# Kernel tuning notes

Hardware: AMD Instinct MI355X
Metric: run time of the kernel (lower is better)

Reference implementation:

```python
import jax, jax.numpy as jnp
import numpy as np

D = 1024; DI = 2048; DS = 16; DTR = 64; K = 4          # mamba dims
HR = 16; DHR = 64                                       # rwkv heads
HA = 32; DHA = 32                                       # attention heads
NM = 6; NR = 4; NT = 2                                  # layer counts
B = 2; L = 1024


def _rms(x, w):
    return x * jax.lax.rsqrt(jnp.mean(x * x, axis=-1, keepdims=True) + 1e-6) * w


def _dwconv(x, w, b):
    # causal depthwise conv over seq; x [B,L,DI], w [K,1,DI]
    xp = jnp.pad(x, ((0, 0), (K - 1, 0), (0, 0)))
    y = jax.lax.conv_general_dilated(xp, w, (1,), 'VALID',
        dimension_numbers=('NWC', 'WIO', 'NWC'), feature_group_count=DI)
    return y + b


def _selective_scan(u, delta, A, Bm, Cm):
    # u,delta [B,L,DI]; A [DI,DS]; Bm,Cm [B,L,DS]
    def step(h, inp):
        u_t, d_t, b_t, c_t = inp
        dA = jnp.exp(d_t[:, :, None] * A)                     # [B,DI,DS]
        h = h * dA + (d_t * u_t)[:, :, None] * b_t[:, None, :]
        return h, jnp.einsum('bds,bs->bd', h, c_t)
    h0 = jnp.zeros((u.shape[0], DI, DS), u.dtype)
    tm = lambda a: jnp.swapaxes(a, 0, 1)                      # time-major
    _, ys = jax.lax.scan(step, h0, (tm(u), tm(delta), tm(Bm), tm(Cm)))
    return jnp.swapaxes(ys, 0, 1)


def _mamba(x, p):
    norm, Win, cw, cb, Wx, Wdt, bdt, Alog, Dp, Wout = p
    xn = _rms(x, norm)
    xz = xn @ Win                                             # [B,L,2*DI]
    xc, z = jnp.split(xz, 2, axis=-1)
    xc = jax.nn.silu(_dwconv(xc, cw, cb))
    xdbl = xc @ Wx                                            # [B,L,DTR+2*DS]
    dt = xdbl[..., :DTR]
    Bm = xdbl[..., DTR:DTR + DS]
    Cm = xdbl[..., DTR + DS:]
    delta = jax.nn.softplus(dt @ Wdt + bdt)                   # [B,L,DI]
    A = -jnp.exp(Alog)
    y = _selective_scan(xc, delta, A, Bm, Cm) + Dp * xc
    y = y * jax.nn.silu(z)
    return x + y @ Wout


def _rwkv(x, p):
    norm, mu, Wr, Wk, Wv, Wo, wlog, u = p
    Bb, Ll = x.shape[0], x.shape[1]
    xn = _rms(x, norm)
    xs = jnp.pad(xn, ((0, 0), (1, 0), (0, 0)))[:, :-1, :]     # token shift
    mix = lambda m: xn * m + xs * (1.0 - m)
    r = (mix(mu[0]) @ Wr).reshape(Bb, Ll, HR, DHR)
    k = (mix(mu[1]) @ Wk).reshape(Bb, Ll, HR, DHR)
    v = (mix(mu[2]) @ Wv).reshape(Bb, Ll, HR, DHR)
    w = jnp.exp(-jnp.exp(wlog))                               # decay in (0,1)
    def step(S, inp):
        r_t, k_t, v_t = inp                                   # [B,HR,DHR]
        kv = jnp.einsum('bhk,bhv->bhkv', k_t, v_t)
        y = jnp.einsum('bhk,bhkv->bhv', r_t, S + u[None, :, :, None] * kv)
        return w[None, :, :, None] * S + kv, y
    S0 = jnp.zeros((Bb, HR, DHR, DHR), x.dtype)
    tm = lambda a: jnp.swapaxes(a, 0, 1)
    _, ys = jax.lax.scan(step, S0, (tm(r), tm(k), tm(v)))
    y = jnp.swapaxes(ys, 0, 1).reshape(Bb, Ll, D)
    return x + y @ Wo


def _mha(x, p):
    Wq, bq, Wk, bk, Wv, bv, Wo, bo = p
    q = jnp.einsum('bld,dhk->blhk', x, Wq) + bq
    k = jnp.einsum('bld,dhk->blhk', x, Wk) + bk
    v = jnp.einsum('bld,dhk->blhk', x, Wv) + bv
    scale = 1.0 / float(np.sqrt(DHA))
    att = jax.nn.softmax(jnp.einsum('blhk,bmhk->bhlm', q, k) * scale, axis=-1)
    o = jnp.einsum('bhlm,bmhk->blhk', att, v)
    return jnp.einsum('blhk,hkd->bld', o, Wo) + bo


def setup_inputs() -> dict:
    key = jax.random.key(0)
    ks = iter(jax.random.split(key, 40))
    nrm = lambda s, sc=0.02: jax.random.normal(next(ks), s, jnp.float32) * sc
    return {
        'x': jax.random.normal(next(ks), (B, L, D), jnp.float32),
        'm_norm': jnp.ones((NM, D), jnp.float32),
        'm_Win': nrm((NM, D, 2 * DI)),
        'm_conv_w': nrm((NM, K, 1, DI)),
        'm_conv_b': jnp.zeros((NM, DI), jnp.float32),
        'm_Wx': nrm((NM, DI, DTR + 2 * DS)),
        'm_Wdt': nrm((NM, DTR, DI)),
        'm_bdt': jnp.full((NM, DI), -4.6, jnp.float32),
        'm_Alog': jnp.broadcast_to(jnp.log(jnp.arange(1, DS + 1, dtype=jnp.float32)), (NM, DI, DS)) + jnp.zeros((NM, DI, DS), jnp.float32),
        'm_D': jnp.ones((NM, DI), jnp.float32),
        'm_Wout': nrm((NM, DI, D)),
        'r_norm': jnp.ones((NR, D), jnp.float32),
        'r_mu': jax.random.uniform(next(ks), (NR, 3, D), jnp.float32),
        'r_Wr': nrm((NR, D, D)), 'r_Wk': nrm((NR, D, D)),
        'r_Wv': nrm((NR, D, D)), 'r_Wo': nrm((NR, D, D)),
        'r_wlog': nrm((NR, HR, DHR), 0.5),
        'r_u': nrm((NR, HR, DHR), 0.5),
        'a_Wq': nrm((NT, D, HA, DHA)), 'a_bq': jnp.zeros((NT, HA, DHA), jnp.float32),
        'a_Wk': nrm((NT, D, HA, DHA)), 'a_bk': jnp.zeros((NT, HA, DHA), jnp.float32),
        'a_Wv': nrm((NT, D, HA, DHA)), 'a_bv': jnp.zeros((NT, HA, DHA), jnp.float32),
        'a_Wo': nrm((NT, HA, DHA, D)), 'a_bo': jnp.zeros((NT, D), jnp.float32),
        'f_W': nrm((3 * D, 3)), 'f_b': jnp.zeros((3,), jnp.float32),
    }


def reference(x, m_norm, m_Win, m_conv_w, m_conv_b, m_Wx, m_Wdt, m_bdt, m_Alog, m_D, m_Wout,
              r_norm, r_mu, r_Wr, r_Wk, r_Wv, r_Wo, r_wlog, r_u,
              a_Wq, a_bq, a_Wk, a_bk, a_Wv, a_bv, a_Wo, a_bo, f_W, f_b):
    m = x
    for i in range(NM):
        m = _mamba(m, (m_norm[i], m_Win[i], m_conv_w[i], m_conv_b[i], m_Wx[i],
                       m_Wdt[i], m_bdt[i], m_Alog[i], m_D[i], m_Wout[i]))
    r = x
    for i in range(NR):
        r = _rwkv(r, (r_norm[i], r_mu[i], r_Wr[i], r_Wk[i], r_Wv[i], r_Wo[i],
                      r_wlog[i], r_u[i]))
    t = x
    for i in range(NT):
        t = _mha(t, (a_Wq[i], a_bq[i], a_Wk[i], a_bk[i], a_Wv[i], a_bv[i],
                     a_Wo[i], a_bo[i]))
    combined = jnp.concatenate([m, r, t], axis=-1)           # [B,L,3*D]
    return jax.nn.softmax(combined @ f_W + f_b, axis=-1)     # [B,L,3]
```

## Files before the change

### kernel.cpp

```cpp
#include <hip/hip_runtime.h>
#include <hip/hip_bf16.h>
#include <cstddef>

#define D_   1024
#define DI_  2048
#define DS_  16
#define DTR_ 64
#define KC_  4
#define HR_  16
#define DHR_ 64
#define HA_  32
#define DHA_ 32
#define NM_  6
#define NR_  4
#define NT_  2
#define B_   2
#define L_   1024
#define NBL  (B_*L_)

typedef __hip_bfloat16 bf16;
typedef __attribute__((ext_vector_type(8))) short short8v;
typedef __attribute__((ext_vector_type(4))) float float4v;

__device__ __forceinline__ float bfbits2f(unsigned short u) {
    return __uint_as_float(((unsigned int)u) << 16);
}
__device__ __forceinline__ float b2f(bf16 x) { return __bfloat162float(x); }
__device__ __forceinline__ unsigned short f2bfbits(float f) {
    bf16 h = __float2bfloat16(f);
    return *reinterpret_cast<unsigned short*>(&h);
}
__device__ __forceinline__ float ldf(const void* p, long i, int bf) {
    if (bf) return bfbits2f(((const unsigned short*)p)[i]);
    return ((const float*)p)[i];
}
__device__ __forceinline__ float softplus_f(float x) {
    return x > 20.f ? x : log1pf(__expf(x));
}
__device__ __forceinline__ float silu_f(float x) {
    return x / (1.f + __expf(-x));
}

__global__ __launch_bounds__(256) void diag_k(float* __restrict__ out, float code)
{
    const int idx = blockIdx.x * 256 + threadIdx.x;
    if (idx < NBL * 3) out[idx] = (idx == 0 ? code : 0.f);
}

__global__ __launch_bounds__(64) void detect_k(const void* __restrict__ x,
                                               int* __restrict__ flag)
{
    const unsigned short* u = (const unsigned short*)x;
    int local = 0;
    for (int i = threadIdx.x; i < 1024; i += 64) {
        const float av = fabsf(bfbits2f(u[i]));
        if (!(av < 1e6f)) local = 1;
    }
    const unsigned long long b = __ballot(local);
    if (threadIdx.x == 0) flag[0] = b ? 0 : 1;
}

#define BM 64
#define BN 64
#define TK 64
#define LDT 72

__global__ __launch_bounds__(256) void gemm_big_k(
    const void* __restrict__ A, int lda, int aDt,
    const void* __restrict__ W, long woff,
    const void* __restrict__ bias, long boff, int hasBias,
    void* __restrict__ C, int ldc, int cDt,
    int N, int K, int act, int acc,
    const int* __restrict__ flagp)
{
    const int bf = *flagp;
    __shared__ short As[128 * LDT];
    __shared__ short Bs[128 * LDT];
    const int bm = blockIdx.y * 128;
    const int bn = blockIdx.x * 128;
    const int tid = threadIdx.x;
    const int lane = tid & 63;
    const int wid = tid >> 6;
    const int wr = wid >> 1, wc = wid & 1;

    const int fc  = lane & 15;
    const int g   = lane >> 4;
    const int fk8 = g << 3;

    const int sa_row = tid >> 1;
    const int sa_k   = (tid & 1) << 5;

    const int sb_n = tid & 127;
    const int sb_k = (tid >> 7) << 5;

    float4v accv[4][4] = {};

    for (int k0 = 0; k0 < K; k0 += TK) {
        if (aDt) {
            const unsigned short* ap = (const unsigned short*)A
                + (size_t)(bm + sa_row) * lda + k0 + sa_k;
            #pragma unroll
            for (int q = 0; q < 4; ++q)
                *(short8v*)&As[sa_row * LDT + sa_k + q * 8] =
                    *(const short8v*)(ap + q * 8);
        } else {
            const float* ap = (const float*)A + (size_t)(bm + sa_row) * lda + k0 + sa_k;
            #pragma unroll
            for (int q = 0; q < 4; ++q) {
                const float4 v0 = *(const float4*)(ap + q * 8);
                const float4 v1 = *(const float4*)(ap + q * 8 + 4);
                short8v t;
                t[0]=(short)f2bfbits(v0.x); t[1]=(short)f2bfbits(v0.y);
                t[2]=(short)f2bfbits(v0.z); t[3]=(short)f2bfbits(v0.w);
                t[4]=(short)f2bfbits(v1.x); t[5]=(short)f2bfbits(v1.y);
                t[6]=(short)f2bfbits(v1.z); t[7]=(short)f2bfbits(v1.w);
                *(short8v*)&As[sa_row * LDT + sa_k + q * 8] = t;
            }
        }
        {
            const long wbase = woff + (long)(k0 + sb_k) * N + (bn + sb_n);
            short tmp[32];
            if (bf) {
                const unsigned short* wp = (const unsigned short*)W;
                #pragma unroll
                for (int j = 0; j < 32; ++j) tmp[j] = (short)wp[wbase + (long)j * N];
            } else {
                const float* wp = (const float*)W;
                #pragma unroll
                for (int j = 0; j < 32; ++j) tmp[j] = (short)f2bfbits(wp[wbase + (long)j * N]);
            }
            #pragma unroll
            for (int q = 0; q < 4; ++q) {
                short8v t;
                #pragma unroll
                for (int e = 0; e < 8; ++e) t[e] = tmp[q * 8 + e];
                *(short8v*)&Bs[sb_n * LDT + sb_k + q * 8] = t;
            }
        }
        __syncthreads();
        #pragma unroll
        for (int ks = 0; ks < TK; ks += 32) {
            short8v af[4], bfr[4];
            #pragma unroll
            for (int mi = 0; mi < 4; ++mi)
                af[mi] = *(const short8v*)&As[(wr * 64 + mi * 16 + fc) * LDT + ks + fk8];
            #pragma unroll
            for (int ni = 0; ni < 4; ++ni)
                bfr[ni] = *(const short8v*)&Bs[(wc * 64 + ni * 16 + fc) * LDT + ks + fk8];
            #pragma unroll
            for (int mi = 0; mi < 4; ++mi)
                #pragma unroll
                for (int ni = 0; ni < 4; ++ni)
                    accv[mi][ni] = __builtin_amdgcn_mfma_f32_16x16x32_bf16(
                        af[mi], bfr[ni], accv[mi][ni], 0, 0, 0);
        }
        __syncthreads();
    }

    const int crow0 = bm + wr * 64 + (g << 2);
    const int ccol0 = bn + wc * 64 + fc;
    #pragma unroll
    for (int ni = 0; ni < 4; ++ni) {
        const int col = ccol0 + ni * 16;
        if (col < N) {
            const float bsv = hasBias ? ldf(bias, boff + col, bf) : 0.f;
            #pragma unroll
            for (int mi = 0; mi < 4; ++mi) {
                #pragma unroll
                for (int j = 0; j < 4; ++j) {
                    const int row = crow0 + mi * 16 + j;
                    float r = accv[mi][ni][j] + bsv;
                    if (act == 1) r = softplus_f(r);
                    if (cDt) {
                        ((bf16*)C)[(size_t)row * ldc + col] = __float2bfloat16(r);
                    } else {
                        float* cp = (float*)C + (size_t)row * ldc + col;
                        if (acc) r += *cp;
                        *cp = r;
                    }
                }
            }
        }
    }
}

__global__ __launch_bounds__(256) void gemm_k(
    const void* __restrict__ A, int lda, int aDt,
    const void* __restrict__ W, long woff,
    const void* __restrict__ bias, long boff, int hasBias,
    void* __restrict__ C, int ldc, int cDt,
    int N, int K, int act, int acc,
    const int* __restrict__ flagp)
{
    const int bf = *flagp;
    __shared__ short As[BM * LDT];
    __shared__ short Bs[BN * LDT];
    const int bm = blockIdx.y * BM;
    const int bn = blockIdx.x * BN;
    const int tid = threadIdx.x;
    const int lane = tid & 63;
    const int wid = tid >> 6;
    const int wr = wid >> 1, wc = wid & 1;

    const int sa_row = tid >> 2;
    const int sa_kq  = (tid & 3) << 4;
    const int sb_col = tid & 63;
    const int sb_kq  = (tid >> 6) << 4;
    const int sb_gn  = bn + sb_col;

    float4v accv[2][2] = {};

    for (int k0 = 0; k0 < K; k0 += TK) {
        {
            short8v a0, a1;
            const size_t aoff = (size_t)(bm + sa_row) * lda + k0 + sa_kq;
            if (aDt) {
                a0 = *(const short8v*)((const unsigned short*)A + aoff);
                a1 = *(const short8v*)((const unsigned short*)A + aoff + 8);
            } else {
                const float* ap = (const float*)A + aoff;
                const float4 v0 = *(const float4*)(ap + 0);
                const float4 v1 = *(const float4*)(ap + 4);
                const float4 v2 = *(const float4*)(ap + 8);
                const float4 v3 = *(const float4*)(ap + 12);
                a0[0]=f2bfbits(v0.x); a0[1]=f2bfbits(v0.y); a0[2]=f2bfbits(v0.z); a0[3]=f2bfbits(v0.w);
                a0[4]=f2bfbits(v1.x); a0[5]=f2bfbits(v1.y); a0[6]=f2bfbits(v1.z); a0[7]=f2bfbits(v1.w);
                a1[0]=f2bfbits(v2.x); a1[1]=f2bfbits(v2.y); a1[2]=f2bfbits(v2.z); a1[3]=f2bfbits(v2.w);
                a1[4]=f2bfbits(v3.x); a1[5]=f2bfbits(v3.y); a1[6]=f2bfbits(v3.z); a1[7]=f2bfbits(v3.w);
            }
            *(short8v*)&As[sa_row * LDT + sa_kq + 0] = a0;
            *(short8v*)&As[sa_row * LDT + sa_kq + 8] = a1;
        }
        {
            short8v b0, b1;
            #pragma unroll
            for (int j = 0; j < 8; ++j) { b0[j] = 0; b1[j] = 0; }
            if (sb_gn < N) {
                const long wbase = woff + (long)(k0 + sb_kq) * N + sb_gn;
                if (bf) {
                    const unsigned short* wp = (const unsigned short*)W;
                    #pragma unroll
                    for (int j = 0; j < 8; ++j) {
                        b0[j] = (short)wp[wbase + (long)j * N];
                        b1[j] = (short)wp[wbase + (long)(j + 8) * N];
                    }
                } else {
                    const float* wp = (const float*)W;
                    #pragma unroll
                    for (int j = 0; j < 8; ++j) {
                        b0[j] = (short)f2bfbits(wp[wbase + (long)j * N]);
                        b1[j] = (short)f2bfbits(wp[wbase + (long)(j + 8) * N]);
                    }
                }
            }
            *(short8v*)&Bs[sb_col * LDT + sb_kq + 0] = b0;
            *(short8v*)&Bs[sb_col * LDT + sb_kq + 8] = b1;
        }
        __syncthreads();
        {
            const int r  = lane & 15;
            const int kb = (lane >> 4) << 3;
            #pragma unroll
            for (int ks = 0; ks < TK; ks += 32) {
                const int kg = ks + kb;
                const short8v a0 = *(const short8v*)&As[(wr*32 +      r) * LDT + kg];
                const short8v a1 = *(const short8v*)&As[(wr*32 + 16 + r) * LDT + kg];
                const short8v b0 = *(const short8v*)&Bs[(wc*32 +      r) * LDT + kg];
                const short8v b1 = *(const short8v*)&Bs[(wc*32 + 16 + r) * LDT + kg];
                accv[0][0] = __builtin_amdgcn_mfma_f32_16x16x32_bf16(a0, b0, accv[0][0], 0, 0, 0);
                accv[0][1] = __builtin_amdgcn_mfma_f32_16x16x32_bf16(a0, b1, accv[0][1], 0, 0, 0);
                accv[1][0] = __builtin_amdgcn_mfma_f32_16x16x32_bf16(a1, b0, accv[1][0], 0, 0, 0);
                accv[1][1] = __builtin_amdgcn_mfma_f32_16x16x32_bf16(a1, b1, accv[1][1], 0, 0, 0);
            }
        }
        __syncthreads();
    }

    const int crow0 = bm + wr * 32 + ((lane >> 4) << 2);
    const int ccol0 = bn + wc * 32 + (lane & 15);
    #pragma unroll
    for (int ni = 0; ni < 2; ++ni) {
        const int col = ccol0 + ni * 16;
        if (col < N) {
            const float bsv = hasBias ? ldf(bias, boff + col, bf) : 0.f;
            #pragma unroll
            for (int mi = 0; mi < 2; ++mi) {
                #pragma unroll
                for (int j = 0; j < 4; ++j) {
                    const int row = crow0 + mi * 16 + j;
                    float r = accv[mi][ni][j] + bsv;
                    if (act == 1) r = softplus_f(r);
                    if (cDt) {
                        ((bf16*)C)[(size_t)row * ldc + col] = __float2bfloat16(r);
                    } else {
                        float* cp = (float*)C + (size_t)row * ldc + col;
                        if (acc) r += *cp;
                        *cp = r;
                    }
                }
            }
        }
    }
}

__global__ __launch_bounds__(256) void cast3_k(const void* __restrict__ x,
    float* __restrict__ a, float* __restrict__ b, float* __restrict__ c,
    const int* __restrict__ flagp)
{
    const int bf = *flagp;
    const int idx = blockIdx.x * 256 + threadIdx.x;
    const float v = ldf(x, idx, bf);
    a[idx] = v; b[idx] = v; c[idx] = v;
}

__global__ __launch_bounds__(256) void rmsnorm_k(const float* __restrict__ x,
    const void* __restrict__ wgt, long woff, float* __restrict__ out,
    const int* __restrict__ flagp)
{
    const int bf = *flagp;
    const int row = blockIdx.x;
    const float* xr = x + (size_t)row * D_;
    float ss = 0.f;
    for (int i = threadIdx.x; i < D_; i += 256) { const float v = xr[i]; ss = fmaf(v, v, ss); }
    #pragma unroll
    for (int msk = 1; msk < 64; msk <<= 1) ss += __shfl_xor(ss, msk);
    __shared__ float red[4];
    if ((threadIdx.x & 63) == 0) red[threadIdx.x >> 6] = ss;
    __syncthreads();
    ss = red[0] + red[1] + red[2] + red[3];
    const float scale = rsqrtf(ss * (1.f / D_) + 1e-6f);
    float* orow = out + (size_t)row * D_;
    for (int i = threadIdx.x; i < D_; i += 256)
        orow[i] = xr[i] * scale * ldf(wgt, woff + i, bf);
}

__global__ __launch_bounds__(256) void conv_silu_k(const bf16* __restrict__ xz,
    const void* __restrict__ cw, long cwoff, const void* __restrict__ cb, long cboff,
    bf16* __restrict__ out, const int* __restrict__ flagp)
{
    const int bf = *flagp;
    const int idx = blockIdx.x * 256 + threadIdx.x;
    const int c = idx & (DI_ - 1);
    const int l = (idx >> 11) & (L_ - 1);
    const int b = idx >> 21;
    float acc = ldf(cb, cboff + c, bf);
    #pragma unroll
    for (int j = 0; j < KC_; ++j) {
        const int ls = l - (KC_ - 1) + j;
        if (ls >= 0)
            acc = fmaf(b2f(xz[((size_t)(b * L_ + ls)) * (2 * DI_) + c]),
                       ldf(cw, cwoff + j * DI_ + c, bf), acc);
    }
    out[idx] = __float2bfloat16(silu_f(acc));
}

#define MS_NCH 16
#define MS_CH  (L_ / MS_NCH)

__global__ __launch_bounds__(256) void mamba_scan_k(
    const bf16* __restrict__ u, const bf16* __restrict__ dlt,
    const float* __restrict__ xdbl, bf16* __restrict__ xz,
    const void* __restrict__ Alog, long aoff, const void* __restrict__ Dp, long doff,
    const int* __restrict__ flagp)
{
    const int bf = *flagp;
    const int bid = ((blockIdx.x & 7) << 9) | (blockIdx.x >> 3);
    const int d = bid & (DI_ - 1);
    const int b = bid >> 11;
    const int s = threadIdx.x & (DS_ - 1);
    const int c = threadIdx.x >> 4;
    const float Av = -__expf(ldf(Alog, aoff + d * DS_ + s, bf));
    const float Dv = ldf(Dp, doff + d, bf);

    __shared__ float Pl[MS_NCH][DS_];
    __shared__ float Sl[MS_NCH][DS_];

    const int l0 = c * MS_CH;

    float P = 1.f, S = 0.f;
    for (int i = 0; i < MS_CH; ++i) {
        const size_t row = (size_t)(b * L_ + l0 + i);
        const float ut = b2f(u[row * DI_ + d]);
        const float dt = b2f(dlt[row * DI_ + d]);
        const float Bv = xdbl[row * 96 + 64 + s];
        const float dA = __expf(dt * Av);
        P *= dA;
        S = fmaf(S, dA, dt * ut * Bv);
    }
    Pl[c][s] = P; Sl[c][s] = S;
    __syncthreads();

    float hs = 0.f;
    for (int cc = 0; cc < c; ++cc) hs = fmaf(hs, Pl[cc][s], Sl[cc][s]);

    for (int i = 0; i < MS_CH; ++i) {
        const size_t row = (size_t)(b * L_ + l0 + i);
        const float ut = b2f(u[row * DI_ + d]);
        const float dt = b2f(dlt[row * DI_ + d]);
        const float Bv = xdbl[row * 96 + 64 + s];
        const float Cv = xdbl[row * 96 + 80 + s];
        const float dA = __expf(dt * Av);
        hs = fmaf(hs, dA, dt * ut * Bv);
        float yp = hs * Cv;
        yp += __shfl_xor(yp, 1, 16);
        yp += __shfl_xor(yp, 2, 16);
        yp += __shfl_xor(yp, 4, 16);
        yp += __shfl_xor(yp, 8, 16);
        if (s == 0) {
            const float z = b2f(xz[row * (2 * DI_) + DI_ + d]);
            xz[row * (2 * DI_) + d] = __float2bfloat16((yp + Dv * ut) * silu_f(z));
        }
    }
}

__global__ __launch_bounds__(256) void rwkv_mix_k(const float* __restrict__ xn,
    const void* __restrict__ mu, long muoff, bf16* __restrict__ o0,
    bf16* __restrict__ o1, bf16* __restrict__ o2, const int* __restrict__ flagp)
{
    const int bf = *flagp;
    const int idx = blockIdx.x * 256 + threadIdx.x;
    const int d = idx & (D_ - 1);
    const int l = (idx >> 10) & (L_ - 1);
    const float cur = xn[idx];
    const float prev = (l > 0) ? xn[idx - D_] : 0.f;
    const float m0 = ldf(mu, muoff + d, bf);
    const float m1 = ldf(mu, muoff + D_ + d, bf);
    const float m2 = ldf(mu, muoff + 2 * D_ + d, bf);
    o0[idx] = __float2bfloat16(cur * m0 + prev * (1.f - m0));
    o1[idx] = __float2bfloat16(cur * m1 + prev * (1.f - m1));
    o2[idx] = __float2bfloat16(cur * m2 + prev * (1.f - m2));
}

#define RW_NCH 16
#define RW_CH  (L_ / RW_NCH)

__global__ __launch_bounds__(1024) void rwkv_scan_k(const bf16* __restrict__ R,
    const bf16* __restrict__ Kb, const bf16* __restrict__ V,
    const void* __restrict__ wlog, long woff, const void* __restrict__ uu, long uoff,
    bf16* __restrict__ Y, const int* __restrict__ flagp)
{
    const int bf = *flagp;
    const int bid = ((blockIdx.x & 7) << 8) | (blockIdx.x >> 3);
    const int v = bid & (DHR_ - 1);
    const int h = (bid >> 6) & (HR_ - 1);
    const int b = bid >> 10;
    const int k = threadIdx.x & 63;
    const int c = threadIdx.x >> 6;
    const float ew = __expf(ldf(wlog, woff + h * DHR_ + k, bf));
    const float w  = __expf(-ew);
    const float wC = __expf(-ew * (float)RW_CH);
    const float uv = ldf(uu, uoff + h * DHR_ + k, bf);

    __shared__ float Se[RW_NCH][64];

    const int l0 = c * RW_CH;

    float S = 0.f;
    for (int i = 0; i < RW_CH; ++i) {
        const size_t off = ((size_t)(b * L_ + l0 + i)) * D_ + h * DHR_;
        const float kk = b2f(Kb[off + k]);
        const float vt = b2f(V[off + v]);
        S = fmaf(w, S, kk * vt);
    }
    Se[c][k] = S;
    __syncthreads();

    S = 0.f;
    for (int cc = 0; cc < c; ++cc) S = fmaf(wC, S, Se[cc][k]);

    for (int i = 0; i < RW_CH; ++i) {
        const size_t off = ((size_t)(b * L_ + l0 + i)) * D_ + h * DHR_;
        const float r  = b2f(R[off + k]);
        const float kk = b2f(Kb[off + k]);
        const float vt = b2f(V[off + v]);
        const float kv = kk * vt;
        float yp = r * fmaf(uv, kv, S);
        S = fmaf(w, S, kv);
        yp += __shfl_xor(yp, 1);
        yp += __shfl_xor(yp, 2);
        yp += __shfl_xor(yp, 4);
        yp += __shfl_xor(yp, 8);
        yp += __shfl_xor(yp, 16);
        yp += __shfl_xor(yp, 32);
        if (k == 0) Y[off + v] = __float2bfloat16(yp);
    }
}

#define LDK 40
#define LDV 72

__global__ __launch_bounds__(256) void mha_attn_k(const bf16* __restrict__ Q,
    const bf16* __restrict__ Kx, const bf16* __restrict__ V, bf16* __restrict__ O)
{
    const int b = blockIdx.z, h = blockIdx.y;
    const int qt = blockIdx.x;
    const int tid = threadIdx.x;
    const int lane = tid & 63;
    const int wid = tid >> 6;

    __shared__ __align__(16) short Ks[64 * LDK];
    __shared__ __align__(16) short Vt[32 * LDV];
    __shared__ __align__(16) short Ps[4][16 * LDV];

    const int fc  = lane & 15;
    const int g   = lane >> 4;
    const int fk8 = g << 3;

    const int q0 = qt * 64 + wid * 16;

    const size_t qoff = ((size_t)(b * L_ + q0 + fc)) * D_ + h * DHA_ + fk8;
    const short8v qf = *(const short8v*)((const unsigned short*)Q + qoff);

    float4v o0 = {}, o1 = {};
    float m[4] = {-1e30f, -1e30f, -1e30f, -1e30f};
    float l[4] = {0.f, 0.f, 0.f, 0.f};
    const float scale = 0.1767766952966369f;

    const int sr = tid >> 2;
    const int sc = (tid & 3) << 3;

    for (int kt = 0; kt < L_; kt += 64) {
        __syncthreads();
        {
            const size_t koff = ((size_t)(b * L_ + kt + sr)) * D_ + h * DHA_ + sc;
            const short8v k8 = *(const short8v*)((const unsigned short*)Kx + koff);
            *(short8v*)&Ks[sr * LDK + sc] = k8;
            const short8v v8 = *(const short8v*)((const unsigned short*)V + koff);
            #pragma unroll
            for (int j = 0; j < 8; ++j)
                Vt[(sc + j) * LDV + sr] = v8[j];
        }
        __syncthreads();

        float4v sv[4];
        #pragma unroll
        for (int nt = 0; nt < 4; ++nt) {
            const short8v kf = *(const short8v*)&Ks[(nt * 16 + fc) * LDK + fk8];
            float4v z = {};
            sv[nt] = __builtin_amdgcn_mfma_f32_16x16x32_bf16(qf, kf, z, 0, 0, 0);
        }

        #pragma unroll
        for (int j = 0; j < 4; ++j) {
            float mt = fmaxf(fmaxf(sv[0][j], sv[1][j]), fmaxf(sv[2][j], sv[3][j])) * scale;
            #pragma unroll
            for (int msk = 1; msk < 16; msk <<= 1) mt = fmaxf(mt, __shfl_xor(mt, msk));
            const float mn = fmaxf(m[j], mt);
            const float corr = __expf(m[j] - mn);
            m[j] = mn;
            float sum = 0.f;
            #pragma unroll
            for (int nt = 0; nt < 4; ++nt) {
                const float p = __expf(fmaf(sv[nt][j], scale, -mn));
                sum += p;
                Ps[wid][(g * 4 + j) * LDV + nt * 16 + fc] = (short)f2bfbits(p);
            }
            #pragma unroll
            for (int msk = 1; msk < 16; msk <<= 1) sum += __shfl_xor(sum, msk);
            l[j] = l[j] * corr + sum;
            o0[j] *= corr;
            o1[j] *= corr;
        }

        #pragma unroll
        for (int kc = 0; kc < 2; ++kc) {
            const short8v pf = *(const short8v*)&Ps[wid][fc * LDV + kc * 32 + fk8];
            const short8v v0 = *(const short8v*)&Vt[(fc) * LDV + kc * 32 + fk8];
            const short8v v1 = *(const short8v*)&Vt[(16 + fc) * LDV + kc * 32 + fk8];
            o0 = __builtin_amdgcn_mfma_f32_16x16x32_bf16(pf, v0, o0, 0, 0, 0);
            o1 = __builtin_amdgcn_mfma_f32_16x16x32_bf16(pf, v1, o1, 0, 0, 0);
        }
    }

    #pragma unroll
    for (int j = 0; j < 4; ++j) {
        const float inv = 1.f / l[j];
        const size_t ooff = ((size_t)(b * L_ + q0 + g * 4 + j)) * D_ + h * DHA_;
        O[ooff + fc]      = __float2bfloat16(o0[j] * inv);
        O[ooff + 16 + fc] = __float2bfloat16(o1[j] * inv);
    }
}

__global__ __launch_bounds__(256) void final_k(const float* __restrict__ m,
    const float* __restrict__ r, const float* __restrict__ t,
    const void* __restrict__ fW, const void* __restrict__ fb,
    float* __restrict__ out, const int* __restrict__ flagp)
{
    const int bf = *flagp;
    const int row = blockIdx.x;
    float p0 = 0.f, p1 = 0.f, p2 = 0.f;
    for (int i = threadIdx.x; i < 3 * D_; i += 256) {
        float v;
        if (i < D_)          v = m[(size_t)row * D_ + i];
        else if (i < 2 * D_) v = r[(size_t)row * D_ + i - D_];
        else                 v = t[(size_t)row * D_ + i - 2 * D_];
        p0 = fmaf(v, ldf(fW, (long)i * 3 + 0, bf), p0);
        p1 = fmaf(v, ldf(fW, (long)i * 3 + 1, bf), p1);
        p2 = fmaf(v, ldf(fW, (long)i * 3 + 2, bf), p2);
    }
    #pragma unroll
    for (int msk = 1; msk < 64; msk <<= 1) {
        p0 += __shfl_xor(p0, msk);
        p1 += __shfl_xor(p1, msk);
        p2 += __shfl_xor(p2, msk);
    }
    __shared__ float red[4][3];
    if ((threadIdx.x & 63) == 0) {
        const int w = threadIdx.x >> 6;
        red[w][0] = p0; red[w][1] = p1; red[w][2] = p2;
    }
    __syncthreads();
    if (threadIdx.x == 0) {
        const float l0 = red[0][0] + red[1][0] + red[2][0] + red[3][0] + ldf(fb, 0, bf);
        const float l1 = red[0][1] + red[1][1] + red[2][1] + red[3][1] + ldf(fb, 1, bf);
        const float l2 = red[0][2] + red[1][2] + red[2][2] + red[3][2] + ldf(fb, 2, bf);
        const float mx = fmaxf(l0, fmaxf(l1, l2));
        const float e0 = __expf(l0 - mx), e1 = __expf(l1 - mx), e2 = __expf(l2 - mx);
        const float inv = 1.f / (e0 + e1 + e2);
        out[row * 3 + 0] = e0 * inv;
        out[row * 3 + 1] = e1 * inv;
        out[row * 3 + 2] = e2 * inv;
    }
}

extern "C" void kernel_launch(void* const* d_in, const int* in_sizes, int n_in,
                              void* d_out, int out_size, void* d_ws, size_t ws_size,
                              hipStream_t stream)
{
    float* out = (float*)d_out;

    static const int expected[29] = {
        2097152, 6144, 25165824, 49152, 12288, 1179648, 786432, 12288,
        196608, 12288, 12582912, 4096, 12288, 4194304, 4194304, 4194304,
        4194304, 4096, 4096, 2097152, 2048, 2097152, 2048, 2097152, 2048,
        2097152, 2048, 9216, 3 };
    int bad = (n_in == 29) ? -1 : 29;
    if (bad < 0)
        for (int i = 0; i < 29; ++i)
            if (in_sizes[i] != expected[i]) { bad = i; break; }
    if (bad >= 0) {
        diag_k<<<24, 256, 0, stream>>>(out, 1000.f + 8.f * bad);
        return;
    }

    const size_t REQ = 64 + 3ull * 8388608 + 8388608 + 16777216 + 8388608 + 786432;
    if (ws_size < REQ) {
        diag_k<<<24, 256, 0, stream>>>(out, 2048.f + (float)(ws_size >> 20));
        return;
    }
    char* base = (char*)d_ws;
    int*   flag = (int*)base;
    float* resM = (float*)(base + 64);
    float* resR = resM + 2097152;
    float* resT = resR + 2097152;
    float* bufN = resT + 2097152;
    bf16*  XZ16 = (bf16*)(bufN + 2097152);
    bf16*  U16  = XZ16 + (size_t)NBL * 4096;
    float* XD   = (float*)(U16 + (size_t)NBL * 2048);

    bf16* q0 = XZ16;
    bf16* q1 = XZ16 + 1 * 2097152;
    bf16* q2 = XZ16 + 2 * 2097152;
    bf16* q3 = XZ16 + 3 * 2097152;
    bf16* u0 = U16;
    bf16* u1 = U16 + 2097152;

    const void* x        = d_in[0];
    const void* m_norm   = d_in[1];
    const void* m_Win    = d_in[2];
    const void* m_conv_w = d_in[3];
    const void* m_conv_b = d_in[4];
    const void* m_Wx     = d_in[5];
    const void* m_Wdt    = d_in[6];
    const void* m_bdt    = d_in[7];
    const void* m_Alog   = d_in[8];
    const void* m_D      = d_in[9];
    const void* m_Wout   = d_in[10];
    const void* r_norm   = d_in[11];
    const void* r_mu     = d_in[12];
    const void* r_Wr     = d_in[13];
    const void* r_Wk     = d_in[14];
    const void* r_Wv     = d_in[15];
    const void* r_Wo     = d_in[16];
    const void* r_wlog   = d_in[17];
    const void* r_u      = d_in[18];
    const void* a_Wq     = d_in[19];
    const void* a_bq     = d_in[20];
    const void* a_Wk     = d_in[21];
    const void* a_bk     = d_in[22];
    const void* a_Wv     = d_in[23];
    const void* a_bv     = d_in[24];
    const void* a_Wo     = d_in[25];
    const void* a_bo     = d_in[26];
    const void* f_W      = d_in[27];
    const void* f_b      = d_in[28];

    auto gemm = [&](const void* A, int lda, int aDt, const void* W, long woff,
                    const void* bias, long boff, int hasBias,
                    void* C, int ldc, int cDt, int N, int K, int act, int acc) {
        if ((N & 127) == 0 && N >= 2048 && (K & 63) == 0) {
            dim3 g(N / 128, NBL / 128);
            gemm_big_k<<<g, 256, 0, stream>>>(A, lda, aDt, W, woff, bias, boff,
                hasBias, C, ldc, cDt, N, K, act, acc, flag);
        } else {
            dim3 g((N + BN - 1) / BN, NBL / BM);
            gemm_k<<<g, 256, 0, stream>>>(A, lda, aDt, W, woff, bias, boff, hasBias,
                                          C, ldc, cDt, N, K, act, acc, flag);
        }
    };

    detect_k<<<1, 64, 0, stream>>>(x, flag);
    cast3_k<<<8192, 256, 0, stream>>>(x, resM, resR, resT, flag);

    for (int i = 0; i < NM_; ++i) {
        rmsnorm_k<<<NBL, 256, 0, stream>>>(resM, m_norm, (long)i * D_, bufN, flag);
        gemm(bufN, D_, 0, m_Win, (long)i * D_ * 2 * DI_, nullptr, 0, 0,
             XZ16, 2 * DI_, 1, 2 * DI_, D_, 0, 0);
        conv_silu_k<<<16384, 256, 0, stream>>>(XZ16, m_conv_w, (long)i * KC_ * DI_,
                                               m_conv_b, (long)i * DI_, U16, flag);
        gemm(U16, DI_, 1, m_Wx, (long)i * DI_ * 96, nullptr, 0, 0,
             XD, 96, 0, 96, DI_, 0, 0);
        gemm(XD, 96, 0, m_Wdt, (long)i * DTR_ * DI_, m_bdt, (long)i * DI_, 1,
             bufN, DI_, 1, DI_, DTR_, 1 , 0);
        mamba_scan_k<<<B_ * DI_, 256, 0, stream>>>(U16, (const bf16*)bufN, XD, XZ16,
            m_Alog, (long)i * DI_ * DS_, m_D, (long)i * DI_, flag);
        gemm(XZ16, 2 * DI_, 1, m_Wout, (long)i * DI_ * D_, nullptr, 0, 0,
             resM, D_, 0, D_, DI_, 0, 1 );
    }

    for (int i = 0; i < NR_; ++i) {
        rmsnorm_k<<<NBL, 256, 0, stream>>>(resR, r_norm, (long)i * D_, bufN, flag);
        rwkv_mix_k<<<8192, 256, 0, stream>>>(bufN, r_mu, (long)i * 3 * D_,
                                             q0, q1, q2, flag);
        gemm(q0, D_, 1, r_Wr, (long)i * D_ * D_, nullptr, 0, 0, u0, D_, 1, D_, D_, 0, 0);
        gemm(q1, D_, 1, r_Wk, (long)i * D_ * D_, nullptr, 0, 0, u1, D_, 1, D_, D_, 0, 0);
        gemm(q2, D_, 1, r_Wv, (long)i * D_ * D_, nullptr, 0, 0, q3, D_, 1, D_, D_, 0, 0);
        rwkv_scan_k<<<B_ * HR_ * DHR_, RW_NCH * 64, 0, stream>>>(u0, u1, q3,
            r_wlog, (long)i * HR_ * DHR_, r_u, (long)i * HR_ * DHR_, q0, flag);
        gemm(q0, D_, 1, r_Wo, (long)i * D_ * D_, nullptr, 0, 0, resR, D_, 0, D_, D_, 0, 1);
    }

    for (int i = 0; i < NT_; ++i) {
        gemm(resT, D_, 0, a_Wq, (long)i * D_ * HA_ * DHA_, a_bq, (long)i * HA_ * DHA_, 1,
             u0, D_, 1, D_, D_, 0, 0);
        gemm(resT, D_, 0, a_Wk, (long)i * D_ * HA_ * DHA_, a_bk, (long)i * HA_ * DHA_, 1,
             u1, D_, 1, D_, D_, 0, 0);
        gemm(resT, D_, 0, a_Wv, (long)i * D_ * HA_ * DHA_, a_bv, (long)i * HA_ * DHA_, 1,
             q3, D_, 1, D_, D_, 0, 0);
        mha_attn_k<<<dim3(L_ / 64, HA_, B_), 256, 0, stream>>>(u0, u1, q3, q0);
        gemm(q0, D_, 1, a_Wo, (long)i * HA_ * DHA_ * D_, a_bo, (long)i * D_, 1,
             resT, D_, 0, D_, HA_ * DHA_, 0, 0 );
    }

    final_k<<<NBL, 256, 0, stream>>>(resM, resR, resT, f_W, f_b, out, flag);
}
```

Measured before the change: 4.086 ms.

## Pre-transpose weights to bf16 N-major so GEMMs load B tiles with vector loads

Adds a transpose-and-convert kernel that writes each weight matrix as bf16 in [N,K] layout before its GEMM, so both GEMM kernels can fill the B tile with contiguous 16-byte loads instead of strided per-element column reads. The rmsnorm output also becomes bf16, which halves A-operand traffic for the downstream GEMMs. The cost is one extra transpose kernel launch and a full weight read/write per GEMM on every call, plus reuse of scratch buffers as transpose targets, which depends on those buffers not being live at that point.

```diff
diff --git a/kernel.cpp b/kernel.cpp
--- a/kernel.cpp
+++ b/kernel.cpp
@@ -60,6 +60,28 @@
     if (threadIdx.x == 0) flag[0] = b ? 0 : 1;
 }
 
+__global__ __launch_bounds__(256) void wcvt_k(const void* __restrict__ W, long woff,
+    int N, int K, bf16* __restrict__ WT, const int* __restrict__ flagp)
+{
+    const int bf = *flagp;
+    __shared__ float t[32][33];
+    const int nt = blockIdx.x << 5;
+    const int kt = blockIdx.y << 5;
+    const int tx = threadIdx.x & 31;
+    const int ty = threadIdx.x >> 5;
+    #pragma unroll
+    for (int i = 0; i < 4; ++i) {
+        const int k = ty + i * 8;
+        t[k][tx] = ldf(W, woff + (long)(kt + k) * N + nt + tx, bf);
+    }
+    __syncthreads();
+    #pragma unroll
+    for (int i = 0; i < 4; ++i) {
+        const int n = ty + i * 8;
+        WT[(size_t)(nt + n) * K + kt + tx] = __float2bfloat16(t[tx][n]);
+    }
+}
+
 #define BM 64
 #define BN 64
 #define TK 64
@@ -67,7 +89,7 @@
 
 __global__ __launch_bounds__(256) void gemm_big_k(
     const void* __restrict__ A, int lda, int aDt,
-    const void* __restrict__ W, long woff,
+    const void* __restrict__ W, long woff, int wDt,
     const void* __restrict__ bias, long boff, int hasBias,
     void* __restrict__ C, int ldc, int cDt,
     int N, int K, int act, int acc,
@@ -89,9 +111,6 @@
 
     const int sa_row = tid >> 1;
     const int sa_k   = (tid & 1) << 5;
-
-    const int sb_n = tid & 127;
-    const int sb_k = (tid >> 7) << 5;
 
     float4v accv[4][4] = {};
 
@@ -117,7 +136,16 @@
                 *(short8v*)&As[sa_row * LDT + sa_k + q * 8] = t;
             }
         }
-        {
+        if (wDt) {
+            const unsigned short* wp = (const unsigned short*)W
+                + (size_t)(bn + sa_row) * K + k0 + sa_k;
+            #pragma unroll
+            for (int q = 0; q < 4; ++q)
+                *(short8v*)&Bs[sa_row * LDT + sa_k + q * 8] =
+                    *(const short8v*)(wp + q * 8);
+        } else {
+            const int sb_n = tid & 127;
+            const int sb_k = (tid >> 7) << 5;
             const long wbase = woff + (long)(k0 + sb_k) * N + (bn + sb_n);
             short tmp[32];
             if (bf) {
@@ -186,7 +214,7 @@
 
 __global__ __launch_bounds__(256) void gemm_k(
     const void* __restrict__ A, int lda, int aDt,
-    const void* __restrict__ W, long woff,
+    const void* __restrict__ W, long woff, int wDt,
     const void* __restrict__ bias, long boff, int hasBias,
     void* __restrict__ C, int ldc, int cDt,
     int N, int K, int act, int acc,
@@ -204,9 +232,6 @@
 
     const int sa_row = tid >> 2;
     const int sa_kq  = (tid & 3) << 4;
-    const int sb_col = tid & 63;
-    const int sb_kq  = (tid >> 6) << 4;
-    const int sb_gn  = bn + sb_col;
 
     float4v accv[2][2] = {};
 
@@ -231,7 +256,23 @@
             *(short8v*)&As[sa_row * LDT + sa_kq + 0] = a0;
             *(short8v*)&As[sa_row * LDT + sa_kq + 8] = a1;
         }
-        {
+        if (wDt) {
+            if (bn + sa_row < N) {
+                const unsigned short* wp = (const unsigned short*)W
+                    + (size_t)(bn + sa_row) * K + k0 + sa_kq;
+                *(short8v*)&Bs[sa_row * LDT + sa_kq + 0] = *(const short8v*)(wp);
+                *(short8v*)&Bs[sa_row * LDT + sa_kq + 8] = *(const short8v*)(wp + 8);
+            } else {
+                short8v z;
+                #pragma unroll
+                for (int e = 0; e < 8; ++e) z[e] = 0;
+                *(short8v*)&Bs[sa_row * LDT + sa_kq + 0] = z;
+                *(short8v*)&Bs[sa_row * LDT + sa_kq + 8] = z;
+            }
+        } else {
+            const int sb_col = tid & 63;
+            const int sb_kq  = (tid >> 6) << 4;
+            const int sb_gn  = bn + sb_col;
             short8v b0, b1;
             #pragma unroll
             for (int j = 0; j < 8; ++j) { b0[j] = 0; b1[j] = 0; }
@@ -314,7 +355,7 @@
 }
 
 __global__ __launch_bounds__(256) void rmsnorm_k(const float* __restrict__ x,
-    const void* __restrict__ wgt, long woff, float* __restrict__ out,
+    const void* __restrict__ wgt, long woff, bf16* __restrict__ out,
     const int* __restrict__ flagp)
 {
     const int bf = *flagp;
@@ -329,9 +370,9 @@
     __syncthreads();
     ss = red[0] + red[1] + red[2] + red[3];
     const float scale = rsqrtf(ss * (1.f / D_) + 1e-6f);
-    float* orow = out + (size_t)row * D_;
+    bf16* orow = out + (size_t)row * D_;
     for (int i = threadIdx.x; i < D_; i += 256)
-        orow[i] = xr[i] * scale * ldf(wgt, woff + i, bf);
+        orow[i] = __float2bfloat16(xr[i] * scale * ldf(wgt, woff + i, bf));
 }
 
 __global__ __launch_bounds__(256) void conv_silu_k(const bf16* __restrict__ xz,
@@ -413,7 +454,7 @@
     }
 }
 
-__global__ __launch_bounds__(256) void rwkv_mix_k(const float* __restrict__ xn,
+__global__ __launch_bounds__(256) void rwkv_mix_k(const bf16* __restrict__ xn,
     const void* __restrict__ mu, long muoff, bf16* __restrict__ o0,
     bf16* __restrict__ o1, bf16* __restrict__ o2, const int* __restrict__ flagp)
 {
@@ -421,8 +462,8 @@
     const int idx = blockIdx.x * 256 + threadIdx.x;
     const int d = idx & (D_ - 1);
     const int l = (idx >> 10) & (L_ - 1);
-    const float cur = xn[idx];
-    const float prev = (l > 0) ? xn[idx - D_] : 0.f;
+    const float cur = b2f(xn[idx]);
+    const float prev = (l > 0) ? b2f(xn[idx - D_]) : 0.f;
     const float m0 = ldf(mu, muoff + d, bf);
     const float m1 = ldf(mu, muoff + D_ + d, bf);
     const float m2 = ldf(mu, muoff + 2 * D_ + d, bf);
@@ -664,6 +705,9 @@
     bf16* q3 = XZ16 + 3 * 2097152;
     bf16* u0 = U16;
     bf16* u1 = U16 + 2097152;
+    bf16* N16 = (bf16*)bufN;
+    bf16* WTb = (bf16*)bufN;
+    bf16* WTu = (bf16*)U16;
 
     const void* x        = d_in[0];
     const void* m_norm   = d_in[1];
@@ -695,17 +739,20 @@
     const void* f_W      = d_in[27];
     const void* f_b      = d_in[28];
 
-    auto gemm = [&](const void* A, int lda, int aDt, const void* W, long woff,
-                    const void* bias, long boff, int hasBias,
-                    void* C, int ldc, int cDt, int N, int K, int act, int acc) {
-        if ((N & 127) == 0 && N >= 2048 && (K & 63) == 0) {
+    auto wcvt = [&](const void* W, long woff, int N, int K, bf16* WT) {
+        wcvt_k<<<dim3(N / 32, K / 32), 256, 0, stream>>>(W, woff, N, K, WT, flag);
+    };
+    auto gemmT = [&](const void* A, int lda, int aDt, const bf16* WT,
+                     const void* bias, long boff, int hasBias,
+                     void* C, int ldc, int cDt, int N, int K, int act, int acc) {
+        if (N >= 2048 && (N & 127) == 0) {
             dim3 g(N / 128, NBL / 128);
-            gemm_big_k<<<g, 256, 0, stream>>>(A, lda, aDt, W, woff, bias, boff,
+            gemm_big_k<<<g, 256, 0, stream>>>(A, lda, aDt, WT, 0, 1, bias, boff,
                 hasBias, C, ldc, cDt, N, K, act, acc, flag);
         } else {
             dim3 g((N + BN - 1) / BN, NBL / BM);
-            gemm_k<<<g, 256, 0, stream>>>(A, lda, aDt, W, woff, bias, boff, hasBias,
-                                          C, ldc, cDt, N, K, act, acc, flag);
+            gemm_k<<<g, 256, 0, stream>>>(A, lda, aDt, WT, 0, 1, bias, boff,
+                hasBias, C, ldc, cDt, N, K, act, acc, flag);
         }
     };
 
@@ -713,43 +760,57 @@
     cast3_k<<<8192, 256, 0, stream>>>(x, resM, resR, resT, flag);
 
     for (int i = 0; i < NM_; ++i) {
-        rmsnorm_k<<<NBL, 256, 0, stream>>>(resM, m_norm, (long)i * D_, bufN, flag);
-        gemm(bufN, D_, 0, m_Win, (long)i * D_ * 2 * DI_, nullptr, 0, 0,
-             XZ16, 2 * DI_, 1, 2 * DI_, D_, 0, 0);
+        rmsnorm_k<<<NBL, 256, 0, stream>>>(resM, m_norm, (long)i * D_, N16, flag);
+        wcvt(m_Win, (long)i * D_ * 2 * DI_, 2 * DI_, D_, WTu);
+        gemmT(N16, D_, 1, WTu, nullptr, 0, 0,
+              XZ16, 2 * DI_, 1, 2 * DI_, D_, 0, 0);
         conv_silu_k<<<16384, 256, 0, stream>>>(XZ16, m_conv_w, (long)i * KC_ * DI_,
                                                m_conv_b, (long)i * DI_, U16, flag);
-        gemm(U16, DI_, 1, m_Wx, (long)i * DI_ * 96, nullptr, 0, 0,
-             XD, 96, 0, 96, DI_, 0, 0);
-        gemm(XD, 96, 0, m_Wdt, (long)i * DTR_ * DI_, m_bdt, (long)i * DI_, 1,
-             bufN, DI_, 1, DI_, DTR_, 1 , 0);
+        wcvt(m_Wx, (long)i * DI_ * 96, 96, DI_, WTb);
+        gemmT(U16, DI_, 1, WTb, nullptr, 0, 0,
+              XD, 96, 0, 96, DI_, 0, 0);
+        {
+            dim3 g(DI_ / 128, NBL / 128);
+            gemm_big_k<<<g, 256, 0, stream>>>(XD, 96, 0, m_Wdt, (long)i * DTR_ * DI_, 0,
+                m_bdt, (long)i * DI_, 1, bufN, DI_, 1, DI_, DTR_, 1 , 0, flag);
+        }
         mamba_scan_k<<<B_ * DI_, 256, 0, stream>>>(U16, (const bf16*)bufN, XD, XZ16,
             m_Alog, (long)i * DI_ * DS_, m_D, (long)i * DI_, flag);
-        gemm(XZ16, 2 * DI_, 1, m_Wout, (long)i * DI_ * D_, nullptr, 0, 0,
-             resM, D_, 0, D_, DI_, 0, 1 );
+        wcvt(m_Wout, (long)i * DI_ * D_, D_, DI_, WTu);
+        gemmT(XZ16, 2 * DI_, 1, WTu, nullptr, 0, 0,
+              resM, D_, 0, D_, DI_, 0, 1 );
     }
 
     for (int i = 0; i < NR_; ++i) {
-        rmsnorm_k<<<NBL, 256, 0, stream>>>(resR, r_norm, (long)i * D_, bufN, flag);
-        rwkv_mix_k<<<8192, 256, 0, stream>>>(bufN, r_mu, (long)i * 3 * D_,
+        rmsnorm_k<<<NBL, 256, 0, stream>>>(resR, r_norm, (long)i * D_, N16, flag);
+        rwkv_mix_k<<<8192, 256, 0, stream>>>(N16, r_mu, (long)i * 3 * D_,
                                              q0, q1, q2, flag);
-        gemm(q0, D_, 1, r_Wr, (long)i * D_ * D_, nullptr, 0, 0, u0, D_, 1, D_, D_, 0, 0);
-        gemm(q1, D_, 1, r_Wk, (long)i * D_ * D_, nullptr, 0, 0, u1, D_, 1, D_, D_, 0, 0);
-        gemm(q2, D_, 1, r_Wv, (long)i * D_ * D_, nullptr, 0, 0, q3, D_, 1, D_, D_, 0, 0);
+        wcvt(r_Wr, (long)i * D_ * D_, D_, D_, WTb);
+        gemmT(q0, D_, 1, WTb, nullptr, 0, 0, u0, D_, 1, D_, D_, 0, 0);
+        wcvt(r_Wk, (long)i * D_ * D_, D_, D_, WTb);
+        gemmT(q1, D_, 1, WTb, nullptr, 0, 0, u1, D_, 1, D_, D_, 0, 0);
+        wcvt(r_Wv, (long)i * D_ * D_, D_, D_, WTb);
+        gemmT(q2, D_, 1, WTb, nullptr, 0, 0, q3, D_, 1, D_, D_, 0, 0);
         rwkv_scan_k<<<B_ * HR_ * DHR_, RW_NCH * 64, 0, stream>>>(u0, u1, q3,
             r_wlog, (long)i * HR_ * DHR_, r_u, (long)i * HR_ * DHR_, q0, flag);
-        gemm(q0, D_, 1, r_Wo, (long)i * D_ * D_, nullptr, 0, 0, resR, D_, 0, D_, D_, 0, 1);
+        wcvt(r_Wo, (long)i * D_ * D_, D_, D_, WTb);
+        gemmT(q0, D_, 1, WTb, nullptr, 0, 0, resR, D_, 0, D_, D_, 0, 1);
     }
 
     for (int i = 0; i < NT_; ++i) {
-        gemm(resT, D_, 0, a_Wq, (long)i * D_ * HA_ * DHA_, a_bq, (long)i * HA_ * DHA_, 1,
-             u0, D_, 1, D_, D_, 0, 0);
-        gemm(resT, D_, 0, a_Wk, (long)i * D_ * HA_ * DHA_, a_bk, (long)i * HA_ * DHA_, 1,
-             u1, D_, 1, D_, D_, 0, 0);
-        gemm(resT, D_, 0, a_Wv, (long)i * D_ * HA_ * DHA_, a_bv, (long)i * HA_ * DHA_, 1,
-             q3, D_, 1, D_, D_, 0, 0);
+        wcvt(a_Wq, (long)i * D_ * HA_ * DHA_, HA_ * DHA_, D_, WTb);
+        gemmT(resT, D_, 0, WTb, a_bq, (long)i * HA_ * DHA_, 1,
+              u0, D_, 1, D_, D_, 0, 0);
+        wcvt(a_Wk, (long)i * D_ * HA_ * DHA_, HA_ * DHA_, D_, WTb);
+        gemmT(resT, D_, 0, WTb, a_bk, (long)i * HA_ * DHA_, 1,
+              u1, D_, 1, D_, D_, 0, 0);
+        wcvt(a_Wv, (long)i * D_ * HA_ * DHA_, HA_ * DHA_, D_, WTb);
+        gemmT(resT, D_, 0, WTb, a_bv, (long)i * HA_ * DHA_, 1,
+              q3, D_, 1, D_, D_, 0, 0);
         mha_attn_k<<<dim3(L_ / 64, HA_, B_), 256, 0, stream>>>(u0, u1, q3, q0);
-        gemm(q0, D_, 1, a_Wo, (long)i * HA_ * DHA_ * D_, a_bo, (long)i * D_, 1,
-             resT, D_, 0, D_, HA_ * DHA_, 0, 0 );
+        wcvt(a_Wo, (long)i * HA_ * DHA_ * D_, D_, HA_ * DHA_, WTb);
+        gemmT(q0, D_, 1, WTb, a_bo, (long)i * D_, 1,
+              resT, D_, 0, D_, HA_ * DHA_, 0, 0 );
     }
 
     final_k<<<NBL, 256, 0, stream>>>(resM, resR, resT, f_W, f_b, out, flag);
```

New measurement: 3.998 ms. 2.2% less time.
